# Performance work log

Hardware: AMD Instinct MI355X
Metric: run time of the kernel (lower is better)

The kernel has to match this reference:

```python
import jax, jax.numpy as jnp
import numpy as np

B, T, FEAT, FUSION, H, C = 128, 64, 4096, 1024, 1024, 2


def setup_inputs() -> dict:
    key = jax.random.key(0)
    ks = jax.random.split(key, 9)
    s_feat = 1.0 / np.sqrt(FEAT)
    s_h = 1.0 / np.sqrt(H)
    return {
        "x": jax.random.normal(ks[0], (B, T, FEAT), jnp.float32),
        "W_feat": jax.random.normal(ks[1], (FUSION, FEAT), jnp.float32) * s_feat,
        "b_feat": jax.random.normal(ks[2], (FUSION,), jnp.float32) * s_feat,
        "W_ih": jax.random.normal(ks[3], (4 * H, FUSION), jnp.float32) * s_h,
        "b_ih": jax.random.normal(ks[4], (4 * H,), jnp.float32) * s_h,
        "W_hh": jax.random.normal(ks[5], (4 * H, H), jnp.float32) * s_h,
        "b_hh": jax.random.normal(ks[6], (4 * H,), jnp.float32) * s_h,
        "W_cls": jax.random.normal(ks[7], (C, H), jnp.float32) * s_h,
        "b_cls": jax.random.normal(ks[8], (C,), jnp.float32) * s_h,
    }


def reference(x, W_feat, b_feat, W_ih, b_ih, W_hh, b_hh, W_cls, b_cls):
    # x: [B, T, FEAT]. Sequential LSTMCell loop expressed as lax.scan over time.
    Hdim = W_hh.shape[1]
    Bb = x.shape[0]
    h0 = jnp.zeros((Bb, Hdim), x.dtype)
    c0 = jnp.zeros((Bb, Hdim), x.dtype)

    def step(carry, x_t):
        h, c = carry
        # feature extractor: Linear + ReLU fusion (dropout = identity in eval)
        f = jax.nn.relu(x_t @ W_feat.T + b_feat)  # [B, FUSION]
        gates = f @ W_ih.T + b_ih + h @ W_hh.T + b_hh  # [B, 4H]
        i, fg, g, o = jnp.split(gates, 4, axis=-1)  # torch LSTMCell gate order
        i = jax.nn.sigmoid(i)
        fg = jax.nn.sigmoid(fg)
        g = jnp.tanh(g)
        o = jax.nn.sigmoid(o)
        c_new = fg * c + i * g
        h_new = o * jnp.tanh(c_new)
        s = h_new @ W_cls.T + b_cls  # [B, 2]
        return (h_new, c_new), s

    xs = jnp.swapaxes(x, 0, 1)  # [T, B, FEAT]
    _, scores = jax.lax.scan(step, (h0, c0), xs)  # [T, B, 2]
    return jnp.swapaxes(scores, 0, 1)  # [B, T, 2]
```

## Files before the change

kernel.cpp:

```cpp
#include <hip/hip_runtime.h>
#include <math.h>


typedef __attribute__((ext_vector_type(8))) short short8v;
typedef __attribute__((ext_vector_type(4))) float f32x4;
typedef unsigned short u16;

#define HF2_BUF 262144
#define HF2_MT  32768

__device__ __forceinline__ u16 f2bf(float f) {
    unsigned u = __builtin_bit_cast(unsigned, f);
    u = (u + 0x7fffu + ((u >> 16) & 1u)) >> 16;
    return (u16)u;
}
__device__ __forceinline__ short f2h(float f) {
    return __builtin_bit_cast(short, (_Float16)f);
}

__global__ void cvt_f16(const float* __restrict__ src, u16* __restrict__ d, int n4) {
    int i = blockIdx.x * blockDim.x + threadIdx.x;
    if (i >= n4) return;
    float4 v = ((const float4*)src)[i];
    ushort4 o;
    o.x = (u16)f2h(v.x); o.y = (u16)f2h(v.y);
    o.z = (u16)f2h(v.z); o.w = (u16)f2h(v.w);
    ((ushort4*)d)[i] = o;
}

template<bool A_PRE16, bool RELU, bool OUT_F16, bool OUT_TMAJOR>
__global__ __launch_bounds__(256)
void gemm_f16(const float* __restrict__ Af,
              const u16* __restrict__ A16, int lda,
              const u16* __restrict__ B16, int ldb,
              const float* __restrict__ bias,
              float* __restrict__ C, u16* __restrict__ C16,
              int ldc, int K)
{
    __shared__ short8v As[8][64];
    __shared__ short8v Bs[8][64];

    const int tid = threadIdx.x;
    const int l   = tid & 63;
    const int w   = tid >> 6;
    const int wm  = w & 1, wn = w >> 1;
    const int bm  = blockIdx.x * 128, bn = blockIdx.y * 128;

    const int sm    = tid >> 2;
    const int sk8   = (tid & 3) * 8;
    const int koct_s = sk8 >> 3;
    const int slane = ((sm & 15) ^ (koct_s << 1)) | (koct_s << 4);
    const int smf   = sm >> 4;
    const int lsw   = ((l & 15) ^ ((l >> 4) << 1)) | (l & 48);

    f32x4 acc[4][4];
#pragma unroll
    for (int i = 0; i < 4; ++i)
#pragma unroll
        for (int j = 0; j < 4; ++j)
#pragma unroll
            for (int r = 0; r < 4; ++r) acc[i][j][r] = 0.f;

    for (int k0 = 0; k0 < K; k0 += 32) {
        if constexpr (A_PRE16) {
            const size_t o0 = (size_t)(bm + sm) * lda + k0 + sk8;
            const size_t o1 = (size_t)(bm + sm + 64) * lda + k0 + sk8;
            As[smf][slane]     = *(const short8v*)(A16 + o0);
            As[smf + 4][slane] = *(const short8v*)(A16 + o1);
        } else {
            float fa[8], fb[8];
            const float* p0 = Af + (size_t)(bm + sm) * lda + k0 + sk8;
            const float* p1 = Af + (size_t)(bm + sm + 64) * lda + k0 + sk8;
            *(float4*)(fa)     = *(const float4*)(p0);
            *(float4*)(fa + 4) = *(const float4*)(p0 + 4);
            *(float4*)(fb)     = *(const float4*)(p1);
            *(float4*)(fb + 4) = *(const float4*)(p1 + 4);
            short8v ha, hb;
#pragma unroll
            for (int e = 0; e < 8; ++e) { ha[e] = f2h(fa[e]); hb[e] = f2h(fb[e]); }
            As[smf][slane]     = ha;
            As[smf + 4][slane] = hb;
        }
        {
            const size_t o0 = (size_t)(bn + sm) * ldb + k0 + sk8;
            const size_t o1 = (size_t)(bn + sm + 64) * ldb + k0 + sk8;
            Bs[smf][slane]     = *(const short8v*)(B16 + o0);
            Bs[smf + 4][slane] = *(const short8v*)(B16 + o1);
        }
        __syncthreads();

        short8v a[4];
#pragma unroll
        for (int i = 0; i < 4; ++i) a[i] = As[wm * 4 + i][lsw];
#pragma unroll
        for (int j = 0; j < 4; ++j) {
            const short8v b = Bs[wn * 4 + j][lsw];
#pragma unroll
            for (int i = 0; i < 4; ++i)
                acc[i][j] = __builtin_amdgcn_mfma_f32_16x16x32_f16(a[i], b, acc[i][j], 0, 0, 0);
        }
        __syncthreads();
    }

    const int row0 = bm + wm * 64 + (l >> 4) * 4;
    const int col0 = bn + wn * 64 + (l & 15);
#pragma unroll
    for (int i = 0; i < 4; ++i) {
#pragma unroll
        for (int j = 0; j < 4; ++j) {
            const int col = col0 + j * 16;
            const float bs = bias[col];
#pragma unroll
            for (int r = 0; r < 4; ++r) {
                const int row = row0 + i * 16 + r;
                float v = acc[i][j][r] + bs;
                if (RELU) v = fmaxf(v, 0.f);
                if (OUT_F16) {
                    C16[(size_t)row * ldc + col] = (u16)f2h(v);
                } else if (OUT_TMAJOR) {
                    const size_t rr = (size_t)(row & 63) * 128 + (row >> 6);
                    C[rr * ldc + col] = v;
                } else {
                    C[(size_t)row * ldc + col] = v;
                }
            }
        }
    }
}

__global__ void pack_whh3(const float* __restrict__ W, char* __restrict__ Wf) {
    int gid = blockIdx.x * blockDim.x + threadIdx.x;
    int l = gid & 63, fid = gid >> 6;
    int kcl = fid & 15, kh = (fid >> 4) & 1, ngrp = (fid >> 5) & 63, g = fid >> 11;
    int n = g * 1024 + ngrp * 16 + (l & 15);
    int k = kh * 512 + kcl * 32 + (l >> 4) * 8;
    const float* src = W + (size_t)n * 1024 + k;
    short8v v16;
#pragma unroll
    for (int e = 0; e < 8; ++e) v16[e] = f2h(src[e]);
    *(short8v*)(Wf + (size_t)fid * 1024 + (size_t)l * 16) = v16;
}

__global__ void out_init(float* __restrict__ out, const float* __restrict__ b_cls) {
    int i = blockIdx.x * blockDim.x + threadIdx.x;
    if (i < 16384) out[i] = b_cls[i & 1];
}

__global__ __launch_bounds__(512)
void lstm_step(const float* __restrict__ Gx,
               const float* __restrict__ b_hh,
               const char*  __restrict__ Wf,
               char*        __restrict__ hfrag,
               float*       __restrict__ c,
               const float* __restrict__ Wc,
               float*       __restrict__ out,
               int t)
{
    __shared__ short8v Hs[64][64];
    __shared__ float gates_s[2][4][32][16];
    __shared__ float h_s[32][16];
    __shared__ float Wc_s[2][16];

    const int tid = threadIdx.x, bid = blockIdx.x;
    const int w = tid >> 6, l = tid & 63;
    const int g = w & 3, kh = w >> 2;
    const int ngrp = bid & 63, mh = bid >> 6;

    if (tid < 32) Wc_s[tid >> 4][tid & 15] =
        Wc[(size_t)(tid >> 4) * 1024 + ngrp * 16 + (tid & 15)];

    const int lhi = l >> 4;
    const int llo = l & 15;

    f32x4 aE0, aO0, aE1, aO1;
#pragma unroll
    for (int r = 0; r < 4; ++r) { aE0[r] = 0.f; aO0[r] = 0.f; aE1[r] = 0.f; aO1[r] = 0.f; }

    if (t > 0) {
        const char* hbase = hfrag + ((t - 1) & 1) * HF2_BUF;
#pragma unroll
        for (int it = 0; it < 8; ++it) {
            const int u  = tid + it * 512;
            const int s  = u >> 6;
            const int ln = u & 63;
            Hs[s][ln] = *(const short8v*)(hbase
                        + (size_t)(2 * mh + (s >> 5)) * HF2_MT
                        + (size_t)(s & 31) * 1024 + (size_t)ln * 16);
        }
        __syncthreads();

        const char* wb = Wf + (size_t)((g * 64 + ngrp) * 2 + kh) * 16384 + (size_t)l * 16;
#pragma unroll
        for (int kcl = 0; kcl < 16; kcl += 2) {
            const short8v b0 = *(const short8v*)(wb + kcl * 1024);
            const short8v b1 = *(const short8v*)(wb + (kcl + 1) * 1024);
            const int kc0 = kh * 16 + kcl;
            aE0 = __builtin_amdgcn_mfma_f32_16x16x32_f16(Hs[kc0][l],      b0, aE0, 0, 0, 0);
            aE1 = __builtin_amdgcn_mfma_f32_16x16x32_f16(Hs[32 + kc0][l], b0, aE1, 0, 0, 0);
            aO0 = __builtin_amdgcn_mfma_f32_16x16x32_f16(Hs[kc0 + 1][l],      b1, aO0, 0, 0, 0);
            aO1 = __builtin_amdgcn_mfma_f32_16x16x32_f16(Hs[32 + kc0 + 1][l], b1, aO1, 0, 0, 0);
        }
    }

#pragma unroll
    for (int r = 0; r < 4; ++r) {
        gates_s[kh][g][lhi * 4 + r][llo]      = aE0[r] + aO0[r];
        gates_s[kh][g][16 + lhi * 4 + r][llo] = aE1[r] + aO1[r];
    }
    __syncthreads();

    {
        const int r  = tid >> 4;
        const int cw = tid & 15;
        const int row = mh * 32 + r;
        const int col = ngrp * 16 + cw;
        float gate[4];
#pragma unroll
        for (int gg = 0; gg < 4; ++gg) {
            const size_t gidx = ((size_t)t * 128 + row) * 4096
                              + (size_t)gg * 1024 + col;
            gate[gg] = gates_s[0][gg][r][cw] + gates_s[1][gg][r][cw]
                     + Gx[gidx] + b_hh[gg * 1024 + col];
        }
        float ig = 1.f / (1.f + __expf(-gate[0]));
        float fg = 1.f / (1.f + __expf(-gate[1]));
        float gg = tanhf(gate[2]);
        float og = 1.f / (1.f + __expf(-gate[3]));
        const size_t cidx = (size_t)row * 1024 + col;
        float cp = (t > 0) ? c[cidx] : 0.f;
        float cn = fg * cp + ig * gg;
        float hn = og * tanhf(cn);
        c[cidx] = cn;
        h_s[r][cw] = hn;

        float s0 = hn * Wc_s[0][cw];
        float s1 = hn * Wc_s[1][cw];
#pragma unroll
        for (int off = 8; off > 0; off >>= 1) {
            s0 += __shfl_xor(s0, off);
            s1 += __shfl_xor(s1, off);
        }
        if (cw == 0) {
            float* o = out + ((size_t)row * 64 + t) * 2;
            atomicAdd(o,     s0);
            atomicAdd(o + 1, s1);
        }
    }
    __syncthreads();

    if (tid < 64) {
        const int idx16  = tid & 15;
        const int koct_h = (tid >> 4) & 1;
        const int mt_l   = (tid >> 5) & 1;
        const int lane   = idx16 | (((ngrp & 1) * 2 + koct_h) << 4);
        short8v v;
#pragma unroll
        for (int e = 0; e < 8; ++e)
            v[e] = f2h(h_s[mt_l * 16 + idx16][koct_h * 8 + e]);
        char* dst = hfrag + (t & 1) * HF2_BUF
                  + (size_t)(2 * mh + mt_l) * HF2_MT
                  + (size_t)(ngrp >> 1) * 1024 + (size_t)lane * 16;
        *(short8v*)dst = v;
    }
}

extern "C" void kernel_launch(void* const* d_in, const int* in_sizes, int n_in,
                              void* d_out, int out_size, void* d_ws, size_t ws_size,
                              hipStream_t stream) {
    const float* x      = (const float*)d_in[0];
    const float* W_feat = (const float*)d_in[1];
    const float* b_feat = (const float*)d_in[2];
    const float* W_ih   = (const float*)d_in[3];
    const float* b_ih   = (const float*)d_in[4];
    const float* W_hh   = (const float*)d_in[5];
    const float* b_hh   = (const float*)d_in[6];
    const float* W_cls  = (const float*)d_in[7];
    const float* b_cls  = (const float*)d_in[8];
    float* out = (float*)d_out;

    char* ws = (char*)d_ws;
    u16*  F16   = (u16*)ws;
    u16*  Wih16 = (u16*)(ws + 16777216);
    u16*  Wf16  = (u16*)(ws + 25165824);
    float* Gx   = (float*)(ws + 33554432);
    char* Wf    = ws;
    char* hfrag = ws + 16777216;
    float* c    = (float*)(ws + 17825792);

    cvt_f16<<<dim3(4096), dim3(256), 0, stream>>>(W_feat, Wf16, 1048576);
    cvt_f16<<<dim3(4096), dim3(256), 0, stream>>>(W_ih, Wih16, 1048576);
    out_init<<<dim3(64), dim3(256), 0, stream>>>(out, b_cls);

    gemm_f16<false, true, true, false>
        <<<dim3(64, 8), 256, 0, stream>>>(
            x, nullptr, 4096, Wf16, 4096, b_feat,
            nullptr, F16, 1024, 4096);

    gemm_f16<true, false, false, true>
        <<<dim3(64, 32), 256, 0, stream>>>(
            nullptr, F16, 1024, Wih16, 1024, b_ih,
            Gx, nullptr, 4096, 1024);

    pack_whh3<<<dim3(2048), dim3(256), 0, stream>>>(W_hh, Wf);

    for (int t = 0; t < 64; ++t) {
        lstm_step<<<dim3(256), dim3(512), 0, stream>>>(
            Gx, b_hh, Wf, hfrag, c, W_cls, out, t);
    }
}
```

Measured before the change: 711.8 us.

## Use direct global-to-LDS loads in GEMMs and LSTM step, pre-convert x to f16

```diff
diff --git a/kernel.cpp b/kernel.cpp
--- a/kernel.cpp
+++ b/kernel.cpp
@@ -9,11 +9,10 @@
 #define HF2_BUF 262144
 #define HF2_MT  32768
 
-__device__ __forceinline__ u16 f2bf(float f) {
-    unsigned u = __builtin_bit_cast(unsigned, f);
-    u = (u + 0x7fffu + ((u >> 16) & 1u)) >> 16;
-    return (u16)u;
-}
+#define GLDS16(g, lp) __builtin_amdgcn_global_load_lds(                      \
+    (const __attribute__((address_space(1))) void*)(g),                      \
+    (__attribute__((address_space(3))) void*)(lp), 16, 0, 0)
+
 __device__ __forceinline__ short f2h(float f) {
     return __builtin_bit_cast(short, (_Float16)f);
 }
@@ -28,10 +27,9 @@
     ((ushort4*)d)[i] = o;
 }
 
-template<bool A_PRE16, bool RELU, bool OUT_F16, bool OUT_TMAJOR>
+template<bool RELU, bool OUT_F16, bool OUT_TMAJOR>
 __global__ __launch_bounds__(256)
-void gemm_f16(const float* __restrict__ Af,
-              const u16* __restrict__ A16, int lda,
+void gemm_f16(const u16* __restrict__ A16, int lda,
               const u16* __restrict__ B16, int ldb,
               const float* __restrict__ bias,
               float* __restrict__ C, u16* __restrict__ C16,
@@ -46,12 +44,12 @@
     const int wm  = w & 1, wn = w >> 1;
     const int bm  = blockIdx.x * 128, bn = blockIdx.y * 128;
 
-    const int sm    = tid >> 2;
-    const int sk8   = (tid & 3) * 8;
-    const int koct_s = sk8 >> 3;
-    const int slane = ((sm & 15) ^ (koct_s << 1)) | (koct_s << 4);
-    const int smf   = sm >> 4;
-    const int lsw   = ((l & 15) ^ ((l >> 4) << 1)) | (l & 48);
+    const int frow = w * 16 + (l & 15);
+    const int koct = (l >> 4) * 8;
+    const u16* gA  = A16 + (size_t)(bm + frow) * lda + koct;
+    const u16* gA2 = gA + (size_t)64 * lda;
+    const u16* gB  = B16 + (size_t)(bn + frow) * ldb + koct;
+    const u16* gB2 = gB + (size_t)64 * ldb;
 
     f32x4 acc[4][4];
 #pragma unroll
@@ -62,39 +60,18 @@
             for (int r = 0; r < 4; ++r) acc[i][j][r] = 0.f;
 
     for (int k0 = 0; k0 < K; k0 += 32) {
-        if constexpr (A_PRE16) {
-            const size_t o0 = (size_t)(bm + sm) * lda + k0 + sk8;
-            const size_t o1 = (size_t)(bm + sm + 64) * lda + k0 + sk8;
-            As[smf][slane]     = *(const short8v*)(A16 + o0);
-            As[smf + 4][slane] = *(const short8v*)(A16 + o1);
-        } else {
-            float fa[8], fb[8];
-            const float* p0 = Af + (size_t)(bm + sm) * lda + k0 + sk8;
-            const float* p1 = Af + (size_t)(bm + sm + 64) * lda + k0 + sk8;
-            *(float4*)(fa)     = *(const float4*)(p0);
-            *(float4*)(fa + 4) = *(const float4*)(p0 + 4);
-            *(float4*)(fb)     = *(const float4*)(p1);
-            *(float4*)(fb + 4) = *(const float4*)(p1 + 4);
-            short8v ha, hb;
-#pragma unroll
-            for (int e = 0; e < 8; ++e) { ha[e] = f2h(fa[e]); hb[e] = f2h(fb[e]); }
-            As[smf][slane]     = ha;
-            As[smf + 4][slane] = hb;
-        }
-        {
-            const size_t o0 = (size_t)(bn + sm) * ldb + k0 + sk8;
-            const size_t o1 = (size_t)(bn + sm + 64) * ldb + k0 + sk8;
-            Bs[smf][slane]     = *(const short8v*)(B16 + o0);
-            Bs[smf + 4][slane] = *(const short8v*)(B16 + o1);
-        }
+        GLDS16(gA  + k0, &As[w][0]);
+        GLDS16(gA2 + k0, &As[w + 4][0]);
+        GLDS16(gB  + k0, &Bs[w][0]);
+        GLDS16(gB2 + k0, &Bs[w + 4][0]);
         __syncthreads();
 
         short8v a[4];
 #pragma unroll
-        for (int i = 0; i < 4; ++i) a[i] = As[wm * 4 + i][lsw];
+        for (int i = 0; i < 4; ++i) a[i] = As[wm * 4 + i][l];
 #pragma unroll
         for (int j = 0; j < 4; ++j) {
-            const short8v b = Bs[wn * 4 + j][lsw];
+            const short8v b = Bs[wn * 4 + j][l];
 #pragma unroll
             for (int i = 0; i < 4; ++i)
                 acc[i][j] = __builtin_amdgcn_mfma_f32_16x16x32_f16(a[i], b, acc[i][j], 0, 0, 0);
@@ -180,12 +157,11 @@
         const char* hbase = hfrag + ((t - 1) & 1) * HF2_BUF;
 #pragma unroll
         for (int it = 0; it < 8; ++it) {
-            const int u  = tid + it * 512;
-            const int s  = u >> 6;
-            const int ln = u & 63;
-            Hs[s][ln] = *(const short8v*)(hbase
+            const int s = w + it * 8;
+            const char* src = hbase
                         + (size_t)(2 * mh + (s >> 5)) * HF2_MT
-                        + (size_t)(s & 31) * 1024 + (size_t)ln * 16);
+                        + (size_t)(s & 31) * 1024 + (size_t)l * 16;
+            GLDS16(src, &Hs[s][0]);
         }
         __syncthreads();
 
@@ -282,23 +258,25 @@
     u16*  F16   = (u16*)ws;
     u16*  Wih16 = (u16*)(ws + 16777216);
     u16*  Wf16  = (u16*)(ws + 25165824);
+    u16*  X16   = (u16*)(ws + 33554432);
     float* Gx   = (float*)(ws + 33554432);
     char* Wf    = ws;
     char* hfrag = ws + 16777216;
     float* c    = (float*)(ws + 17825792);
 
+    cvt_f16<<<dim3(32768), dim3(256), 0, stream>>>(x, X16, 8388608);
     cvt_f16<<<dim3(4096), dim3(256), 0, stream>>>(W_feat, Wf16, 1048576);
     cvt_f16<<<dim3(4096), dim3(256), 0, stream>>>(W_ih, Wih16, 1048576);
     out_init<<<dim3(64), dim3(256), 0, stream>>>(out, b_cls);
 
-    gemm_f16<false, true, true, false>
+    gemm_f16<true, true, false>
         <<<dim3(64, 8), 256, 0, stream>>>(
-            x, nullptr, 4096, Wf16, 4096, b_feat,
+            X16, 4096, Wf16, 4096, b_feat,
             nullptr, F16, 1024, 4096);
 
-    gemm_f16<true, false, false, true>
+    gemm_f16<false, false, true>
         <<<dim3(64, 32), 256, 0, stream>>>(
-            nullptr, F16, 1024, Wih16, 1024, b_ih,
+            F16, 1024, Wih16, 1024, b_ih,
             Gx, nullptr, 4096, 1024);
 
     pack_whh3<<<dim3(2048), dim3(256), 0, stream>>>(W_hh, Wf);
```

Result: slower. 783.8 us (+10.1%).

## Store input-gate projections as gate-interleaved fp16 for vectorized step loads

Applied to the files above, without the earlier changes.

```diff
diff --git a/kernel.cpp b/kernel.cpp
--- a/kernel.cpp
+++ b/kernel.cpp
@@ -9,13 +9,11 @@
 #define HF2_BUF 262144
 #define HF2_MT  32768
 
-__device__ __forceinline__ u16 f2bf(float f) {
-    unsigned u = __builtin_bit_cast(unsigned, f);
-    u = (u + 0x7fffu + ((u >> 16) & 1u)) >> 16;
-    return (u16)u;
-}
 __device__ __forceinline__ short f2h(float f) {
     return __builtin_bit_cast(short, (_Float16)f);
+}
+__device__ __forceinline__ float h2f(u16 h) {
+    return (float)__builtin_bit_cast(_Float16, (short)h);
 }
 
 __global__ void cvt_f16(const float* __restrict__ src, u16* __restrict__ d, int n4) {
@@ -28,7 +26,7 @@
     ((ushort4*)d)[i] = o;
 }
 
-template<bool A_PRE16, bool RELU, bool OUT_F16, bool OUT_TMAJOR>
+template<bool A_PRE16, bool RELU, bool OUT_F16, bool OUT_GI>
 __global__ __launch_bounds__(256)
 void gemm_f16(const float* __restrict__ Af,
               const u16* __restrict__ A16, int lda,
@@ -117,9 +115,9 @@
                 if (RELU) v = fmaxf(v, 0.f);
                 if (OUT_F16) {
                     C16[(size_t)row * ldc + col] = (u16)f2h(v);
-                } else if (OUT_TMAJOR) {
+                } else if (OUT_GI) {
                     const size_t rr = (size_t)(row & 63) * 128 + (row >> 6);
-                    C[rr * ldc + col] = v;
+                    C16[rr * 4096 + (size_t)(col & 1023) * 4 + (col >> 10)] = (u16)f2h(v);
                 } else {
                     C[(size_t)row * ldc + col] = v;
                 }
@@ -147,7 +145,7 @@
 }
 
 __global__ __launch_bounds__(512)
-void lstm_step(const float* __restrict__ Gx,
+void lstm_step(const u16* __restrict__ Gxi,
                const float* __restrict__ b_hh,
                const char*  __restrict__ Wf,
                char*        __restrict__ hfrag,
@@ -214,14 +212,15 @@
         const int cw = tid & 15;
         const int row = mh * 32 + r;
         const int col = ngrp * 16 + cw;
+        const ushort4 gv = *(const ushort4*)(Gxi
+                          + ((size_t)t * 128 + row) * 4096 + (size_t)col * 4);
         float gate[4];
-#pragma unroll
-        for (int gg = 0; gg < 4; ++gg) {
-            const size_t gidx = ((size_t)t * 128 + row) * 4096
-                              + (size_t)gg * 1024 + col;
-            gate[gg] = gates_s[0][gg][r][cw] + gates_s[1][gg][r][cw]
-                     + Gx[gidx] + b_hh[gg * 1024 + col];
-        }
+        gate[0] = h2f(gv.x); gate[1] = h2f(gv.y);
+        gate[2] = h2f(gv.z); gate[3] = h2f(gv.w);
+#pragma unroll
+        for (int gg = 0; gg < 4; ++gg)
+            gate[gg] += gates_s[0][gg][r][cw] + gates_s[1][gg][r][cw]
+                      + b_hh[gg * 1024 + col];
         float ig = 1.f / (1.f + __expf(-gate[0]));
         float fg = 1.f / (1.f + __expf(-gate[1]));
         float gg = tanhf(gate[2]);
@@ -282,7 +281,7 @@
     u16*  F16   = (u16*)ws;
     u16*  Wih16 = (u16*)(ws + 16777216);
     u16*  Wf16  = (u16*)(ws + 25165824);
-    float* Gx   = (float*)(ws + 33554432);
+    u16*  Gxi   = (u16*)(ws + 33554432);
     char* Wf    = ws;
     char* hfrag = ws + 16777216;
     float* c    = (float*)(ws + 17825792);
@@ -299,12 +298,12 @@
     gemm_f16<true, false, false, true>
         <<<dim3(64, 32), 256, 0, stream>>>(
             nullptr, F16, 1024, Wih16, 1024, b_ih,
-            Gx, nullptr, 4096, 1024);
+            nullptr, Gxi, 4096, 1024);
 
     pack_whh3<<<dim3(2048), dim3(256), 0, stream>>>(W_hh, Wf);
 
     for (int t = 0; t < 64; ++t) {
         lstm_step<<<dim3(256), dim3(512), 0, stream>>>(
-            Gx, b_hh, Wf, hfrag, c, W_cls, out, t);
-    }
-}
+            Gxi, b_hh, Wf, hfrag, c, W_cls, out, t);
+    }
+}
```

After: 725.3 us. About the same (+1.9%).
